# Kernel tuning notes

Hardware: AMD Instinct MI355X
Metric: run time of the kernel (lower is better)

## Reference

```python
import jax, jax.numpy as jnp
import numpy as np

B, LQ, LK = 4, 1024, 2048
DQ, DK, DV, D = 1024, 512, 512, 1024
H = 16
HD = D // H
EPS = 1e-5


def setup_inputs() -> dict:
    key = jax.random.key(0)
    ks = jax.random.split(key, 12)
    s = lambda fan: 1.0 / np.sqrt(fan)
    return {
        "query": jax.random.normal(ks[0], (B, LQ, DQ), jnp.float32),
        "key": jax.random.normal(ks[1], (B, LK, DK), jnp.float32),
        "value": jax.random.normal(ks[2], (B, LK, DV), jnp.float32),
        "key_padding_mask": jnp.ones((B, LK), jnp.int32),
        "Wq": jax.random.normal(ks[3], (DQ, D), jnp.float32) * s(DQ),
        "bq": jnp.zeros((D,), jnp.float32),
        "Wk": jax.random.normal(ks[4], (DK, D), jnp.float32) * s(DK),
        "bk": jnp.zeros((D,), jnp.float32),
        "Wv": jax.random.normal(ks[5], (DV, D), jnp.float32) * s(DV),
        "bv": jnp.zeros((D,), jnp.float32),
        "Wo": jax.random.normal(ks[6], (D, D), jnp.float32) * s(D),
        "bo": jnp.zeros((D,), jnp.float32),
        "ln_g": jnp.ones((D,), jnp.float32),
        "ln_b": jnp.zeros((D,), jnp.float32),
    }


def _layer_norm(x, g, b):
    mu = jnp.mean(x, axis=-1, keepdims=True)
    var = jnp.mean(jnp.square(x - mu), axis=-1, keepdims=True)
    return (x - mu) * jax.lax.rsqrt(var + EPS) * g + b


def reference(query, key, value, key_padding_mask, Wq, bq, Wk, bk, Wv, bv, Wo, bo, ln_g, ln_b):
    residual = query
    qn = _layer_norm(query, ln_g, ln_b)
    # projections -> [B, L, H, HD]
    q = (qn @ Wq + bq).reshape(B, LQ, H, HD)
    k = (key @ Wk + bk).reshape(B, LK, H, HD)
    v = (value @ Wv + bv).reshape(B, LK, H, HD)
    scale = HD ** -0.5
    # scores [B, H, Lq, Lk]
    scores = jnp.einsum("bqhd,bkhd->bhqk", q, k) * scale
    mask = (key_padding_mask != 0)[:, None, None, :]  # True = keep
    scores = jnp.where(mask, scores, -jnp.inf)
    attn = jax.nn.softmax(scores, axis=-1)
    # dropout is identity in eval mode
    ctx = jnp.einsum("bhqk,bkhd->bqhd", attn, v).reshape(B, LQ, D)
    out = ctx @ Wo + bo
    return out + residual
```

## Files before the change

### kernel.cpp

```cpp
#include <hip/hip_runtime.h>
#include <hip/hip_bf16.h>
#include <stdint.h>

#define Bn 4
#define LQ 1024
#define LK 2048
#define Dm 1024
#define Hn 16
#define HD 64

typedef __attribute__((ext_vector_type(4))) float f32x4;
typedef __attribute__((ext_vector_type(16))) float f32x16;
typedef __attribute__((ext_vector_type(8))) short bf16x8;

__device__ __forceinline__ ushort f2bf(float f) {
  union { float f; uint32_t u; } v; v.f = f;
  uint32_t r = v.u + 0x7FFF + ((v.u >> 16) & 1);
  return (ushort)(r >> 16);
}

__device__ __forceinline__ uint32_t cvt_pk_bf16(float lo, float hi) {
  uint32_t r;
  asm("v_cvt_pk_bf16_f32 %0, %1, %2" : "=v"(r) : "v"(lo), "v"(hi));
  return r;
}

__device__ __forceinline__ float exp2v(float x) {
  float r;
  asm("v_exp_f32 %0, %1" : "=v"(r) : "v"(x));
  return r;
}

__device__ __forceinline__ void gload16(const void* g, void* lds) {
  __builtin_amdgcn_global_load_lds(
      (const __attribute__((address_space(1))) void*)g,
      (__attribute__((address_space(3))) void*)lds, 16, 0, 0);
}

__device__ __forceinline__ void wait_vm0_barrier() {
  asm volatile("s_waitcnt vmcnt(0)" ::: "memory");
  __builtin_amdgcn_s_barrier();
}

__device__ __forceinline__ void wait_all_barrier() {
  asm volatile("s_waitcnt vmcnt(0) lgkmcnt(0)" ::: "memory");
  __builtin_amdgcn_s_barrier();
}

__device__ __forceinline__ void wait_lgkm0_barrier() {
  asm volatile("s_waitcnt lgkmcnt(0)" ::: "memory");
  __builtin_amdgcn_s_barrier();
}

__global__ __launch_bounds__(256) void transpose_cast_kernel(
    const float* __restrict__ W, ushort* __restrict__ Wt, int K, int N) {
  __shared__ float tile[64][65];
  int k0 = blockIdx.x * 64, n0 = blockIdx.y * 64;
  int tx = threadIdx.x & 63, ty = threadIdx.x >> 6;
#pragma unroll
  for (int i = 0; i < 16; ++i) {
    int r = ty + i * 4;
    tile[r][tx] = W[(size_t)(k0 + r) * N + n0 + tx];
  }
  __syncthreads();
#pragma unroll
  for (int i = 0; i < 16; ++i) {
    int r = ty + i * 4;
    Wt[(size_t)(n0 + r) * K + k0 + tx] = f2bf(tile[tx][r]);
  }
}

__global__ __launch_bounds__(256) void cast_bf16_kernel(
    const float4* __restrict__ in, ushort4* __restrict__ out, int n4) {
  int i = blockIdx.x * blockDim.x + threadIdx.x;
  int stride = gridDim.x * blockDim.x;
  for (; i < n4; i += stride) {
    float4 v = in[i];
    out[i] = make_ushort4(f2bf(v.x), f2bf(v.y), f2bf(v.z), f2bf(v.w));
  }
}

__global__ __launch_bounds__(256) void ln_kernel(
    const float* __restrict__ x, const float* __restrict__ g,
    const float* __restrict__ b, ushort* __restrict__ y) {
  int row = blockIdx.x;
  const float4* xr = (const float4*)(x + (size_t)row * 1024);
  float4 v = xr[threadIdx.x];
  float s1 = v.x + v.y + v.z + v.w;
  float s2 = v.x * v.x + v.y * v.y + v.z * v.z + v.w * v.w;
#pragma unroll
  for (int off = 32; off > 0; off >>= 1) {
    s1 += __shfl_down(s1, off);
    s2 += __shfl_down(s2, off);
  }
  __shared__ float r1[4], r2[4];
  int w = threadIdx.x >> 6, lane = threadIdx.x & 63;
  if (lane == 0) { r1[w] = s1; r2[w] = s2; }
  __syncthreads();
  s1 = r1[0] + r1[1] + r1[2] + r1[3];
  s2 = r2[0] + r2[1] + r2[2] + r2[3];
  float mu = s1 * (1.0f / 1024.0f);
  float var = s2 * (1.0f / 1024.0f) - mu * mu;
  float rstd = rsqrtf(var + 1e-5f);
  float4 gv = ((const float4*)g)[threadIdx.x];
  float4 bv = ((const float4*)b)[threadIdx.x];
  ushort4 o;
  o.x = f2bf((v.x - mu) * rstd * gv.x + bv.x);
  o.y = f2bf((v.y - mu) * rstd * gv.y + bv.y);
  o.z = f2bf((v.z - mu) * rstd * gv.z + bv.z);
  o.w = f2bf((v.w - mu) * rstd * gv.w + bv.w);
  ((ushort4*)(y + (size_t)row * 1024))[threadIdx.x] = o;
}

__global__ __launch_bounds__(512) void qkv_gemm_kernel(
    const ushort* __restrict__ qn, const ushort* __restrict__ WqT,
    const float* __restrict__ bq, ushort* __restrict__ Qb,
    const ushort* __restrict__ keyb, const ushort* __restrict__ WkT,
    const float* __restrict__ bk, ushort* __restrict__ Kb,
    const ushort* __restrict__ valb, const ushort* __restrict__ WvT,
    const float* __restrict__ bv, ushort* __restrict__ Vt, float qscale) {
  __shared__ ushort As[2][128 * 64];
  __shared__ ushort Bs[2][128 * 64];

  int o = blockIdx.x;
  int logical = (o & 7) * 160 + (o >> 3);
  const ushort* A; const ushort* Bt; const float* bias; ushort* out;
  int K, bx, by, epi; float osc = 1.0f;
  if (logical < 256) {
    A = qn; Bt = WqT; bias = bq; out = Qb; K = 1024; epi = 0;
    osc = qscale; bx = logical & 7; by = logical >> 3;
  } else if (logical < 768) {
    int i = logical - 256;
    A = keyb; Bt = WkT; bias = bk; out = Kb; K = 512; epi = 0;
    bx = i & 7; by = i >> 3;
  } else {
    int i = logical - 768;
    A = valb; Bt = WvT; bias = bv; out = Vt; K = 512; epi = 1;
    bx = i & 7; by = i >> 3;
  }
  const int N = 1024;
  const int m0 = by * 128, n0 = bx * 128;

  const int t = threadIdx.x;
  const int lane = t & 63;
  const int w = t >> 6;
  const int wm = w >> 2, wn = w & 3;
  const int l31 = lane & 31, hl = lane >> 5;

  f32x16 acc[2] = {};

  const ushort* Ap[2];
  const ushort* Bp[2];
#pragma unroll
  for (int i = 0; i < 2; ++i) {
    int c = t + i * 512;
    int r = c >> 3, x = ((c & 7) ^ (r & 7)) * 8;
    Ap[i] = A + (size_t)(m0 + r) * K + x;
    Bp[i] = Bt + (size_t)(n0 + r) * K + x;
  }

  auto stage = [&](int buf, int kt) {
    gload16(Ap[0] + kt, (char*)As[buf] + (size_t)t * 16);
    gload16(Ap[1] + kt, (char*)As[buf] + (size_t)(t + 512) * 16);
    gload16(Bp[0] + kt, (char*)Bs[buf] + (size_t)t * 16);
    gload16(Bp[1] + kt, (char*)Bs[buf] + (size_t)(t + 512) * 16);
  };

  stage(0, 0);

  int cur = 0;
  for (int kt = 0; kt < K; kt += 64) {
    if (kt + 64 < K) {
      stage(cur ^ 1, kt + 64);
      asm volatile("s_waitcnt vmcnt(4)" ::: "memory");
    } else {
      asm volatile("s_waitcnt vmcnt(0)" ::: "memory");
    }
    __builtin_amdgcn_s_barrier();

    bf16x8 af[2][4], bfr[4];
#pragma unroll
    for (int m = 0; m < 2; ++m) {
      int row = wm * 64 + m * 32 + l31;
      const char* ar = (const char*)As[cur] + row * 128;
      int rs = row & 7;
#pragma unroll
      for (int kc = 0; kc < 4; ++kc)
        af[m][kc] = *(const bf16x8*)(ar + ((kc * 2 + hl) ^ rs) * 16);
    }
    {
      int row = wn * 32 + l31;
      const char* br = (const char*)Bs[cur] + row * 128;
      int rs = row & 7;
#pragma unroll
      for (int kc = 0; kc < 4; ++kc)
        bfr[kc] = *(const bf16x8*)(br + ((kc * 2 + hl) ^ rs) * 16);
    }
#pragma unroll
    for (int kc = 0; kc < 4; ++kc)
#pragma unroll
      for (int m = 0; m < 2; ++m)
        acc[m] = __builtin_amdgcn_mfma_f32_32x32x16_bf16(af[m][kc], bfr[kc], acc[m], 0, 0, 0);

    wait_lgkm0_barrier();
    cur ^= 1;
  }

  const int col = n0 + wn * 32 + l31;
  const float bias_v = bias[col];

#pragma unroll
  for (int m = 0; m < 2; ++m) {
    int rbase = m0 + wm * 64 + m * 32 + hl * 4;
#pragma unroll
    for (int rq = 0; rq < 4; ++rq) {
      int row0 = rbase + rq * 8;
      if (epi == 1) {
        int bb = row0 >> 11;
        int key = row0 & 2047;
        int h = col >> 6, hd = col & 63;
        ushort4 pk;
        pk.x = f2bf(acc[m][rq * 4 + 0] + bias_v);
        pk.y = f2bf(acc[m][rq * 4 + 1] + bias_v);
        pk.z = f2bf(acc[m][rq * 4 + 2] + bias_v);
        pk.w = f2bf(acc[m][rq * 4 + 3] + bias_v);
        *(ushort4*)(out + ((size_t)((bb * 16 + h) * 64 + hd)) * 2048 + key) = pk;
      } else {
#pragma unroll
        for (int j = 0; j < 4; ++j) {
          int row = row0 + j;
          float v = (acc[m][rq * 4 + j] + bias_v) * osc;
          out[(size_t)row * N + col] = f2bf(v);
        }
      }
    }
  }
}

__global__ __launch_bounds__(512) void oproj_gemm_kernel(
    const ushort* __restrict__ A, const ushort* __restrict__ Bt,
    const float* __restrict__ bias, float* __restrict__ Cout,
    const float* __restrict__ residual, int M, int N, int K) {
  __shared__ ushort As[2][128 * 64];
  __shared__ ushort Bs[2][128 * 64];
  const int t = threadIdx.x;
  const int lane = t & 63;
  const int w = t >> 6;
  const int wm = w >> 2, wn = w & 3;
  const int m0 = blockIdx.y * 128, n0 = blockIdx.x * 128;
  const int l31 = lane & 31, hl = lane >> 5;

  f32x16 acc[2] = {};

  const ushort* Ap[2];
  const ushort* Bp[2];
#pragma unroll
  for (int i = 0; i < 2; ++i) {
    int c = t + i * 512;
    int r = c >> 3, x = ((c & 7) ^ (r & 7)) * 8;
    Ap[i] = A + (size_t)(m0 + r) * K + x;
    Bp[i] = Bt + (size_t)(n0 + r) * K + x;
  }

  auto stage = [&](int buf, int kt) {
    gload16(Ap[0] + kt, (char*)As[buf] + (size_t)t * 16);
    gload16(Ap[1] + kt, (char*)As[buf] + (size_t)(t + 512) * 16);
    gload16(Bp[0] + kt, (char*)Bs[buf] + (size_t)t * 16);
    gload16(Bp[1] + kt, (char*)Bs[buf] + (size_t)(t + 512) * 16);
  };

  stage(0, 0);

  int cur = 0;
  for (int kt = 0; kt < K; kt += 64) {
    if (kt + 64 < K) {
      stage(cur ^ 1, kt + 64);
      asm volatile("s_waitcnt vmcnt(4)" ::: "memory");
    } else {
      asm volatile("s_waitcnt vmcnt(0)" ::: "memory");
    }
    __builtin_amdgcn_s_barrier();

    bf16x8 af[2][4], bfr[4];
#pragma unroll
    for (int m = 0; m < 2; ++m) {
      int row = wm * 64 + m * 32 + l31;
      const char* ar = (const char*)As[cur] + row * 128;
      int rs = row & 7;
#pragma unroll
      for (int kc = 0; kc < 4; ++kc)
        af[m][kc] = *(const bf16x8*)(ar + ((kc * 2 + hl) ^ rs) * 16);
    }
    {
      int row = wn * 32 + l31;
      const char* br = (const char*)Bs[cur] + row * 128;
      int rs = row & 7;
#pragma unroll
      for (int kc = 0; kc < 4; ++kc)
        bfr[kc] = *(const bf16x8*)(br + ((kc * 2 + hl) ^ rs) * 16);
    }
#pragma unroll
    for (int kc = 0; kc < 4; ++kc)
#pragma unroll
      for (int m = 0; m < 2; ++m)
        acc[m] = __builtin_amdgcn_mfma_f32_32x32x16_bf16(af[m][kc], bfr[kc], acc[m], 0, 0, 0);

    wait_lgkm0_barrier();
    cur ^= 1;
  }

  const int col = n0 + wn * 32 + l31;
  const float bias_v = bias[col];

#pragma unroll
  for (int m = 0; m < 2; ++m) {
    int rbase = m0 + wm * 64 + m * 32 + hl * 4;
#pragma unroll
    for (int rq = 0; rq < 4; ++rq) {
      int row0 = rbase + rq * 8;
#pragma unroll
      for (int j = 0; j < 4; ++j) {
        size_t idx = (size_t)(row0 + j) * N + col;
        Cout[idx] = acc[m][rq * 4 + j] + bias_v + residual[idx];
      }
    }
  }
}

__global__ __launch_bounds__(256) void attn_kernel(
    const ushort* __restrict__ Qb, const ushort* __restrict__ Kb,
    const ushort* __restrict__ Vt, const int* __restrict__ mask,
    ushort* __restrict__ ctx) {
  __shared__ __align__(16) char smem[128 + 2 * 16384];
  int* tilevalid = (int*)smem;
  char* KsBase = smem + 128;
  char* VsBase = smem + 128 + 16384;

  const int t = threadIdx.x, lane = t & 63, w = t >> 6;
  const int l31 = lane & 31, hl = lane >> 5;
  int o = blockIdx.x;
  int logical = (o & 7) * 64 + (o >> 3);
  const int b = logical >> 7;
  const int hh = (logical >> 3) & 15;
  const int q0 = (logical & 7) * 128;
  const int* maskp = mask + b * 2048;

  const int cA = t, cB = t + 256;
  const int rA = cA >> 3, rB = cB >> 3;
  const int xA = ((cA & 7) ^ (rA & 7)) * 8, xB = ((cB & 7) ^ (rB & 7)) * 8;
  const ushort* kpA = Kb + ((size_t)(b * 2048 + rA)) * 1024 + hh * 64 + xA;
  const ushort* kpB = Kb + ((size_t)(b * 2048 + rB)) * 1024 + hh * 64 + xB;
  const ushort* vpA = Vt + ((size_t)((b * 16 + hh) * 64 + rA)) * 2048 + xA;
  const ushort* vpB = Vt + ((size_t)((b * 16 + hh) * 64 + rB)) * 2048 + xB;

  auto stageKV = [&](int buf) {
    char* kd = KsBase + buf * 8192;
    char* vd = VsBase + buf * 8192;
    gload16(kpA, kd + cA * 16);
    gload16(kpB, kd + cB * 16);
    gload16(vpA, vd + cA * 16);
    gload16(vpB, vd + cB * 16);
  };

  if (t < 32) tilevalid[t] = 1;
  __syncthreads();
  stageKV(0);
  {
    const int* mp = maskp + t * 8;
    int ok = 1;
#pragma unroll
    for (int j = 0; j < 8; ++j) ok &= (mp[j] != 0) ? 1 : 0;
    atomicAnd(&tilevalid[t >> 3], ok);
  }

  bf16x8 qf[4];
  {
    int qrow = q0 + w * 32 + l31;
    const ushort* qp = Qb + ((size_t)(b * 1024 + qrow)) * 1024 + hh * 64 + hl * 8;
    qf[0] = *(const bf16x8*)(qp);
    qf[1] = *(const bf16x8*)(qp + 16);
    qf[2] = *(const bf16x8*)(qp + 32);
    qf[3] = *(const bf16x8*)(qp + 48);
  }

  const int rs = l31 & 7;
  int lo[2][2][4];
#pragma unroll
  for (int bu = 0; bu < 2; ++bu)
#pragma unroll
    for (int r2 = 0; r2 < 2; ++r2)
#pragma unroll
      for (int kc = 0; kc < 4; ++kc)
        lo[bu][r2][kc] = 128 + bu * 8192 + (r2 * 32 + l31) * 128 + (((kc * 2 + hl) ^ rs) * 16);

  f32x16 o_acc[2] = {};
  float m_run = -1e30f, l_run = 0.0f;

  wait_all_barrier();

  auto body = [&](const int CUR, int TILE) __attribute__((always_inline)) {
    if (TILE + 1 < 32) {
      kpA += 64 * 1024; kpB += 64 * 1024; vpA += 64; vpB += 64;
      stageKV(CUR ^ 1);
    }

    f32x16 sacc[2] = {};
    __builtin_amdgcn_s_setprio(1);
#pragma unroll
    for (int kb = 0; kb < 2; ++kb)
#pragma unroll
      for (int kc = 0; kc < 4; ++kc) {
        bf16x8 kf = *(const bf16x8*)(smem + lo[CUR][kb][kc]);
        sacc[kb] = __builtin_amdgcn_mfma_f32_32x32x16_bf16(kf, qf[kc], sacc[kb], 0, 0, 0);
      }
    __builtin_amdgcn_s_setprio(0);

    int allv = __builtin_amdgcn_readfirstlane(tilevalid[TILE]);
    if (!allv) {
      const int* mrow = maskp + TILE * 64 + 4 * hl;
#pragma unroll
      for (int kb = 0; kb < 2; ++kb)
#pragma unroll
        for (int rq = 0; rq < 4; ++rq) {
          int4 mv = *(const int4*)(mrow + kb * 32 + rq * 8);
          sacc[kb][rq * 4 + 0] = mv.x ? sacc[kb][rq * 4 + 0] : -1e30f;
          sacc[kb][rq * 4 + 1] = mv.y ? sacc[kb][rq * 4 + 1] : -1e30f;
          sacc[kb][rq * 4 + 2] = mv.z ? sacc[kb][rq * 4 + 2] : -1e30f;
          sacc[kb][rq * 4 + 3] = mv.w ? sacc[kb][rq * 4 + 3] : -1e30f;
        }
    }

    float tm = fmaxf(sacc[0][0], sacc[0][1]);
#pragma unroll
    for (int r = 2; r < 16; r += 2) tm = fmaxf(fmaxf(tm, sacc[0][r]), sacc[0][r + 1]);
#pragma unroll
    for (int r = 0; r < 16; r += 2) tm = fmaxf(fmaxf(tm, sacc[1][r]), sacc[1][r + 1]);
    {
      float s1 = tm, s2 = tm;
      asm("v_permlane32_swap_b32 %0, %1" : "+v"(s1), "+v"(s2));
      tm = fmaxf(tm, hl ? s1 : s2);
    }

    if (__any(tm - m_run > 11.5f)) {
      float mn = fmaxf(m_run, tm);
      float al = exp2v(m_run - mn);
      m_run = mn;
      l_run *= al;
#pragma unroll
      for (int df = 0; df < 2; ++df)
#pragma unroll
        for (int r = 0; r < 16; ++r) o_acc[df][r] *= al;
    }

    float psA = 0.0f, psB = 0.0f;
    uint32_t cpk[2][8];
#pragma unroll
    for (int kb = 0; kb < 2; ++kb)
#pragma unroll
      for (int rr = 0; rr < 8; ++rr) {
        float pa = exp2v(sacc[kb][2 * rr] - m_run);
        float pb = exp2v(sacc[kb][2 * rr + 1] - m_run);
        psA += pa; psB += pb;
        cpk[kb][rr] = cvt_pk_bf16(pa, pb);
      }
    float psum = psA + psB;
    {
      float s1 = psum, s2 = psum;
      asm("v_permlane32_swap_b32 %0, %1" : "+v"(s1), "+v"(s2));
      psum += hl ? s1 : s2;
    }
    l_run += psum;

    __builtin_amdgcn_s_setprio(1);
#pragma unroll
    for (int ks = 0; ks < 4; ++ks) {
      const int kb = ks >> 1, ci = (ks & 1) * 4;
      uint32_t a0 = cpk[kb][ci],     b0 = cpk[kb][ci + 2];
      uint32_t a1 = cpk[kb][ci + 1], b1 = cpk[kb][ci + 3];
      asm("v_permlane32_swap_b32 %0, %1" : "+v"(a0), "+v"(b0));
      asm("v_permlane32_swap_b32 %0, %1" : "+v"(a1), "+v"(b1));
      union { uint32_t u[4]; bf16x8 v; } pb_;
      pb_.u[0] = a0; pb_.u[1] = a1; pb_.u[2] = b0; pb_.u[3] = b1;
#pragma unroll
      for (int df = 0; df < 2; ++df) {
        bf16x8 vf = *(const bf16x8*)(smem + lo[CUR][df][ks] + 16384);
        o_acc[df] = __builtin_amdgcn_mfma_f32_32x32x16_bf16(vf, pb_.v, o_acc[df], 0, 0, 0);
      }
    }
    __builtin_amdgcn_s_setprio(0);

    wait_vm0_barrier();
  };

  for (int tile = 0; tile < 32; tile += 2) {
    body(0, tile);
    body(1, tile + 1);
  }

  float inv = l_run > 0.0f ? 1.0f / l_run : 0.0f;
  char* ob = KsBase + w * 4096;
#pragma unroll
  for (int df = 0; df < 2; ++df)
#pragma unroll
    for (int rq = 0; rq < 4; ++rq) {
      ushort4 pk;
      pk.x = f2bf(o_acc[df][rq * 4 + 0] * inv);
      pk.y = f2bf(o_acc[df][rq * 4 + 1] * inv);
      pk.z = f2bf(o_acc[df][rq * 4 + 2] * inv);
      pk.w = f2bf(o_acc[df][rq * 4 + 3] * inv);
      *(ushort4*)(ob + l31 * 128 + (((df * 4 + rq) ^ (l31 & 7)) * 16) + hl * 8) = pk;
    }
  asm volatile("s_waitcnt lgkmcnt(0)" ::: "memory");
#pragma unroll
  for (int i = 0; i < 4; ++i) {
    int q = (lane >> 3) + i * 8;
    int ch = lane & 7;
    uint4 v = *(const uint4*)(ob + q * 128 + ((ch ^ (q & 7)) * 16));
    int qrow = q0 + w * 32 + q;
    *(uint4*)(ctx + ((size_t)(b * 1024 + qrow)) * 1024 + hh * 64 + ch * 8) = v;
  }
}

extern "C" void kernel_launch(void* const* d_in, const int* in_sizes, int n_in,
                              void* d_out, int out_size, void* d_ws, size_t ws_size,
                              hipStream_t stream) {
  const float* query = (const float*)d_in[0];
  const float* key   = (const float*)d_in[1];
  const float* value = (const float*)d_in[2];
  const int*   mask  = (const int*)d_in[3];
  const float* Wq = (const float*)d_in[4];
  const float* bq = (const float*)d_in[5];
  const float* Wk = (const float*)d_in[6];
  const float* bk = (const float*)d_in[7];
  const float* Wv = (const float*)d_in[8];
  const float* bv = (const float*)d_in[9];
  const float* Wo = (const float*)d_in[10];
  const float* bo = (const float*)d_in[11];
  const float* ln_g = (const float*)d_in[12];
  const float* ln_b = (const float*)d_in[13];
  float* out = (float*)d_out;

  char* p = (char*)d_ws;
  auto alloc = [&](size_t elems) { ushort* r = (ushort*)p; p += elems * 2; return r; };
  ushort* WqT  = alloc((size_t)1024 * 1024);
  ushort* WkT  = alloc((size_t)1024 * 512);
  ushort* WvT  = alloc((size_t)1024 * 512);
  ushort* WoT  = alloc((size_t)1024 * 1024);
  ushort* qn   = alloc((size_t)4096 * 1024);
  ushort* keyb = alloc((size_t)8192 * 512);
  ushort* valb = alloc((size_t)8192 * 512);
  ushort* Qb   = alloc((size_t)4096 * 1024);
  ushort* Kb   = alloc((size_t)8192 * 1024);
  ushort* Vt   = alloc((size_t)8192 * 1024);
  ushort* ctx  = alloc((size_t)4096 * 1024);
  (void)ws_size; (void)in_sizes; (void)n_in; (void)out_size;

  const float QSCALE = 0.125f * 1.44269504f;

  dim3 blk(256);
  dim3 blk5(512);
  transpose_cast_kernel<<<dim3(16, 16), blk, 0, stream>>>(Wq, WqT, 1024, 1024);
  transpose_cast_kernel<<<dim3(8, 16),  blk, 0, stream>>>(Wk, WkT, 512, 1024);
  transpose_cast_kernel<<<dim3(8, 16),  blk, 0, stream>>>(Wv, WvT, 512, 1024);
  transpose_cast_kernel<<<dim3(16, 16), blk, 0, stream>>>(Wo, WoT, 1024, 1024);
  cast_bf16_kernel<<<dim3(1024), blk, 0, stream>>>((const float4*)key,   (ushort4*)keyb, (8192 * 512) / 4);
  cast_bf16_kernel<<<dim3(1024), blk, 0, stream>>>((const float4*)value, (ushort4*)valb, (8192 * 512) / 4);
  ln_kernel<<<dim3(4096), blk, 0, stream>>>(query, ln_g, ln_b, qn);

  qkv_gemm_kernel<<<dim3(1280), blk5, 0, stream>>>(
      qn, WqT, bq, Qb, keyb, WkT, bk, Kb, valb, WvT, bv, Vt, QSCALE);

  attn_kernel<<<dim3(512), blk, 0, stream>>>(Qb, Kb, Vt, mask, ctx);

  oproj_gemm_kernel<<<dim3(8, 32), blk5, 0, stream>>>(ctx, WoT, bo, out, query, 4096, 1024, 1024);
}
```

Baseline: 162.2 us.

## Use K=32 tiles with k-major LDS layout in QKV and output GEMMs

Both GEMM kernels now stage 32-wide K slices instead of 64, storing them in LDS in a k-chunk-major layout rather than the XOR-swizzled row-major one. This halves shared memory per block, which should raise occupancy. The output-projection GEMM also moves to 256-thread blocks with 128x64 tiles, doubling the grid for better CU coverage. In exchange there are twice as many barrier-synchronised iterations with fewer MFMAs each. The new unswizzled layout may also cause LDS bank conflicts.

```diff
diff --git a/kernel.cpp b/kernel.cpp
--- a/kernel.cpp
+++ b/kernel.cpp
@@ -119,8 +119,7 @@
     const float* __restrict__ bk, ushort* __restrict__ Kb,
     const ushort* __restrict__ valb, const ushort* __restrict__ WvT,
     const float* __restrict__ bv, ushort* __restrict__ Vt, float qscale) {
-  __shared__ ushort As[2][128 * 64];
-  __shared__ ushort Bs[2][128 * 64];
+  __shared__ __align__(16) char SM[32768];
 
   int o = blockIdx.x;
   int logical = (o & 7) * 160 + (o >> 3);
@@ -149,55 +148,45 @@
 
   f32x16 acc[2] = {};
 
-  const ushort* Ap[2];
-  const ushort* Bp[2];
-#pragma unroll
-  for (int i = 0; i < 2; ++i) {
-    int c = t + i * 512;
-    int r = c >> 3, x = ((c & 7) ^ (r & 7)) * 8;
-    Ap[i] = A + (size_t)(m0 + r) * K + x;
-    Bp[i] = Bt + (size_t)(n0 + r) * K + x;
-  }
+  const int srow = t & 127, sks = t >> 7;
+  const ushort* Ap = A + (size_t)(m0 + srow) * K + sks * 8;
+  const ushort* Bp = Bt + (size_t)(n0 + srow) * K + sks * 8;
 
   auto stage = [&](int buf, int kt) {
-    gload16(Ap[0] + kt, (char*)As[buf] + (size_t)t * 16);
-    gload16(Ap[1] + kt, (char*)As[buf] + (size_t)(t + 512) * 16);
-    gload16(Bp[0] + kt, (char*)Bs[buf] + (size_t)t * 16);
-    gload16(Bp[1] + kt, (char*)Bs[buf] + (size_t)(t + 512) * 16);
+    gload16(Ap + kt, SM + buf * 8192 + (size_t)t * 16);
+    gload16(Bp + kt, SM + 16384 + buf * 8192 + (size_t)t * 16);
   };
 
   stage(0, 0);
 
   int cur = 0;
-  for (int kt = 0; kt < K; kt += 64) {
-    if (kt + 64 < K) {
-      stage(cur ^ 1, kt + 64);
-      asm volatile("s_waitcnt vmcnt(4)" ::: "memory");
+  for (int kt = 0; kt < K; kt += 32) {
+    if (kt + 32 < K) {
+      stage(cur ^ 1, kt + 32);
+      asm volatile("s_waitcnt vmcnt(2)" ::: "memory");
     } else {
       asm volatile("s_waitcnt vmcnt(0)" ::: "memory");
     }
     __builtin_amdgcn_s_barrier();
 
-    bf16x8 af[2][4], bfr[4];
+    bf16x8 af[2][2], bfr[2];
+    const char* Ab = SM + cur * 8192;
+    const char* Bb = SM + 16384 + cur * 8192;
 #pragma unroll
     for (int m = 0; m < 2; ++m) {
       int row = wm * 64 + m * 32 + l31;
-      const char* ar = (const char*)As[cur] + row * 128;
-      int rs = row & 7;
-#pragma unroll
-      for (int kc = 0; kc < 4; ++kc)
-        af[m][kc] = *(const bf16x8*)(ar + ((kc * 2 + hl) ^ rs) * 16);
+#pragma unroll
+      for (int kc = 0; kc < 2; ++kc)
+        af[m][kc] = *(const bf16x8*)(Ab + ((kc * 2 + hl) * 128 + row) * 16);
     }
     {
       int row = wn * 32 + l31;
-      const char* br = (const char*)Bs[cur] + row * 128;
-      int rs = row & 7;
-#pragma unroll
-      for (int kc = 0; kc < 4; ++kc)
-        bfr[kc] = *(const bf16x8*)(br + ((kc * 2 + hl) ^ rs) * 16);
-    }
-#pragma unroll
-    for (int kc = 0; kc < 4; ++kc)
+#pragma unroll
+      for (int kc = 0; kc < 2; ++kc)
+        bfr[kc] = *(const bf16x8*)(Bb + ((kc * 2 + hl) * 128 + row) * 16);
+    }
+#pragma unroll
+    for (int kc = 0; kc < 2; ++kc)
 #pragma unroll
       for (int m = 0; m < 2; ++m)
         acc[m] = __builtin_amdgcn_mfma_f32_32x32x16_bf16(af[m][kc], bfr[kc], acc[m], 0, 0, 0);
@@ -237,70 +226,60 @@
   }
 }
 
-__global__ __launch_bounds__(512) void oproj_gemm_kernel(
+__global__ __launch_bounds__(256) void oproj_gemm_kernel(
     const ushort* __restrict__ A, const ushort* __restrict__ Bt,
     const float* __restrict__ bias, float* __restrict__ Cout,
     const float* __restrict__ residual, int M, int N, int K) {
-  __shared__ ushort As[2][128 * 64];
-  __shared__ ushort Bs[2][128 * 64];
+  __shared__ __align__(16) char SM[24576];
   const int t = threadIdx.x;
   const int lane = t & 63;
   const int w = t >> 6;
-  const int wm = w >> 2, wn = w & 3;
-  const int m0 = blockIdx.y * 128, n0 = blockIdx.x * 128;
+  const int wm = w >> 1, wn = w & 1;
+  const int m0 = blockIdx.y * 128, n0 = blockIdx.x * 64;
   const int l31 = lane & 31, hl = lane >> 5;
 
   f32x16 acc[2] = {};
 
-  const ushort* Ap[2];
-  const ushort* Bp[2];
-#pragma unroll
-  for (int i = 0; i < 2; ++i) {
-    int c = t + i * 512;
-    int r = c >> 3, x = ((c & 7) ^ (r & 7)) * 8;
-    Ap[i] = A + (size_t)(m0 + r) * K + x;
-    Bp[i] = Bt + (size_t)(n0 + r) * K + x;
-  }
+  const ushort* Ap0 = A + (size_t)(m0 + (t & 127)) * K + (t >> 7) * 8;
+  const ushort* Ap1 = A + (size_t)(m0 + ((t + 256) & 127)) * K + ((t + 256) >> 7) * 8;
+  const ushort* Bp  = Bt + (size_t)(n0 + (t & 63)) * K + (t >> 6) * 8;
 
   auto stage = [&](int buf, int kt) {
-    gload16(Ap[0] + kt, (char*)As[buf] + (size_t)t * 16);
-    gload16(Ap[1] + kt, (char*)As[buf] + (size_t)(t + 512) * 16);
-    gload16(Bp[0] + kt, (char*)Bs[buf] + (size_t)t * 16);
-    gload16(Bp[1] + kt, (char*)Bs[buf] + (size_t)(t + 512) * 16);
+    gload16(Ap0 + kt, SM + buf * 8192 + (size_t)t * 16);
+    gload16(Ap1 + kt, SM + buf * 8192 + (size_t)(t + 256) * 16);
+    gload16(Bp + kt, SM + 16384 + buf * 4096 + (size_t)t * 16);
   };
 
   stage(0, 0);
 
   int cur = 0;
-  for (int kt = 0; kt < K; kt += 64) {
-    if (kt + 64 < K) {
-      stage(cur ^ 1, kt + 64);
-      asm volatile("s_waitcnt vmcnt(4)" ::: "memory");
+  for (int kt = 0; kt < K; kt += 32) {
+    if (kt + 32 < K) {
+      stage(cur ^ 1, kt + 32);
+      asm volatile("s_waitcnt vmcnt(3)" ::: "memory");
     } else {
       asm volatile("s_waitcnt vmcnt(0)" ::: "memory");
     }
     __builtin_amdgcn_s_barrier();
 
-    bf16x8 af[2][4], bfr[4];
+    bf16x8 af[2][2], bfr[2];
+    const char* Ab = SM + cur * 8192;
+    const char* Bb = SM + 16384 + cur * 4096;
 #pragma unroll
     for (int m = 0; m < 2; ++m) {
       int row = wm * 64 + m * 32 + l31;
-      const char* ar = (const char*)As[cur] + row * 128;
-      int rs = row & 7;
-#pragma unroll
-      for (int kc = 0; kc < 4; ++kc)
-        af[m][kc] = *(const bf16x8*)(ar + ((kc * 2 + hl) ^ rs) * 16);
+#pragma unroll
+      for (int kc = 0; kc < 2; ++kc)
+        af[m][kc] = *(const bf16x8*)(Ab + ((kc * 2 + hl) * 128 + row) * 16);
     }
     {
       int row = wn * 32 + l31;
-      const char* br = (const char*)Bs[cur] + row * 128;
-      int rs = row & 7;
-#pragma unroll
-      for (int kc = 0; kc < 4; ++kc)
-        bfr[kc] = *(const bf16x8*)(br + ((kc * 2 + hl) ^ rs) * 16);
-    }
-#pragma unroll
-    for (int kc = 0; kc < 4; ++kc)
+#pragma unroll
+      for (int kc = 0; kc < 2; ++kc)
+        bfr[kc] = *(const bf16x8*)(Bb + ((kc * 2 + hl) * 64 + row) * 16);
+    }
+#pragma unroll
+    for (int kc = 0; kc < 2; ++kc)
 #pragma unroll
       for (int m = 0; m < 2; ++m)
         acc[m] = __builtin_amdgcn_mfma_f32_32x32x16_bf16(af[m][kc], bfr[kc], acc[m], 0, 0, 0);
@@ -572,5 +551,5 @@
 
   attn_kernel<<<dim3(512), blk, 0, stream>>>(Qb, Kb, Vt, mask, ctx);
 
-  oproj_gemm_kernel<<<dim3(8, 32), blk5, 0, stream>>>(ctx, WoT, bo, out, query, 4096, 1024, 1024);
-}
+  oproj_gemm_kernel<<<dim3(16, 32), blk, 0, stream>>>(ctx, WoT, bo, out, query, 4096, 1024, 1024);
+}
```

After: 202.3 us. 24.7% more time.
